# Kernel tuning notes

Hardware: AMD Instinct MI355X
Metric: run time of the kernel (lower is better)

## Reference

```python
import jax, jax.numpy as jnp
import numpy as np

B, T = 64, 512
D_CH, D_W = 50, 300
D_IN = D_CH + D_W          # 350, GRU input dim
H = 700                    # hidden_nums
U = H // 2                 # 350, units per direction


def _gru_dir(x, mask, Wx, Wh, b, reverse):
    """Keras GRU (reset_after=True, gate order z,r,h) over time axis.
    x: [B,T,D_IN], mask: [B,T] bool, Wx: [D_IN,3U], Wh: [U,3U], b: [2,3U].
    Masked steps carry the previous state (Keras masking semantics).
    Returns hidden states [B,T,U] aligned to input time order."""
    xg = jnp.einsum('btd,dg->btg', x, Wx) + b[0]  # [B,T,3U] precomputed input gates

    def step(h, inp):
        xg_t, m = inp                      # [B,3U], [B]
        hg = h @ Wh + b[1]                 # [B,3U]
        z = jax.nn.sigmoid(xg_t[:, :U] + hg[:, :U])
        r = jax.nn.sigmoid(xg_t[:, U:2 * U] + hg[:, U:2 * U])
        hh = jnp.tanh(xg_t[:, 2 * U:] + r * hg[:, 2 * U:])
        h_new = z * h + (1.0 - z) * hh
        h = jnp.where(m[:, None], h_new, h)
        return h, h

    h0 = jnp.zeros((x.shape[0], U), x.dtype)
    _, ys = jax.lax.scan(step, h0, (xg.transpose(1, 0, 2), mask.T), reverse=reverse)
    return ys.transpose(1, 0, 2)           # [B,T,U]


def setup_inputs() -> dict:
    key = jax.random.key(0)
    ks = jax.random.split(key, 12)
    char_embedding = jax.random.normal(ks[0], (B, T, D_CH), jnp.float32)
    word_embedding = jax.random.normal(ks[1], (B, T, D_W), jnp.float32)
    sequence_length = jax.random.randint(ks[2], (B,), 1, T + 1, jnp.int32)
    mask = jnp.arange(T)[None, :] < sequence_length[:, None]  # right-padded bool mask

    def glorot(k, shape):
        lim = np.sqrt(6.0 / (shape[0] + shape[1]))
        return jax.random.uniform(k, shape, jnp.float32, -lim, lim)

    W_z = glorot(ks[3], (2, H))
    W_q = glorot(ks[4], (2, H))
    Wx_f = glorot(ks[5], (D_IN, 3 * U))
    Wh_f = glorot(ks[6], (U, 3 * U))
    b_f = jnp.zeros((2, 3 * U), jnp.float32)
    Wx_b = glorot(ks[7], (D_IN, 3 * U))
    Wh_b = glorot(ks[8], (U, 3 * U))
    b_b = jnp.zeros((2, 3 * U), jnp.float32)
    return {
        'char_embedding': char_embedding, 'word_embedding': word_embedding,
        'sequence_length': sequence_length, 'mask': mask,
        'W_z': W_z, 'W_q': W_q,
        'Wx_f': Wx_f, 'Wh_f': Wh_f, 'b_f': b_f,
        'Wx_b': Wx_b, 'Wh_b': Wh_b, 'b_b': b_b,
    }


def reference(char_embedding, word_embedding, sequence_length, mask,
              W_z, W_q, Wx_f, Wh_f, b_f, Wx_b, Wh_b, b_b):
    x = jnp.concatenate([char_embedding, word_embedding], axis=-1)   # [B,T,350]
    h_fw = _gru_dir(x, mask, Wx_f, Wh_f, b_f, reverse=False)
    h_bw = _gru_dir(x, mask, Wx_b, Wh_b, b_b, reverse=True)
    hidden_states = jnp.concatenate([h_fw, h_bw], axis=-1)           # [B,T,700]
    z_T = jax.nn.softmax(jnp.einsum('bth,ch->btc', hidden_states, W_z), axis=-1)
    z_S = jax.nn.softmax(jnp.einsum('bth,ch->btc', hidden_states, W_q), axis=-1)
    return (z_T, z_S, hidden_states)
```

## Files before the change

kernel.cpp:

```cpp
#include <hip/hip_runtime.h>
#include <hip/hip_bf16.h>
#include <math.h>

#define BB   64
#define TT   512
#define UU   350
#define GG   1050
#define DCH  50
#define DWD  300
#define DIN  350
#define CT   64
#define NCH  8

#define NSLICE 22
#define UPB    16
#define NBG    4
#define BPG    16

#define FLAGS_OFF 0
#define WHT_ROW   352
#define WHT_OFF   1024
#define WHT_BYTES (2*GG*WHT_ROW*4)
#define XG_OFF    (WHT_OFF + WHT_BYTES)

__global__ __launch_bounds__(256) void wht_kernel(
    const float* __restrict__ Whf, const float* __restrict__ Whb,
    float* __restrict__ WhT)
{
    int idx = blockIdx.x * 256 + threadIdx.x;
    if (idx >= 2 * WHT_ROW * GG) return;
    int dir = idx / (WHT_ROW * GG);
    int r   = idx % (WHT_ROW * GG);
    int u   = r / GG;
    int g   = r % GG;
    const float* src = dir ? Whb : Whf;
    float v = (u < UU) ? src[u * GG + g] : 0.f;
    WhT[((size_t)dir * GG + g) * WHT_ROW + u] = v;
}

__global__ __launch_bounds__(256) void xg_gemm_kernel(
    const float* __restrict__ ce, const float* __restrict__ we,
    const float* __restrict__ Wxf, const float* __restrict__ Wxb,
    const float* __restrict__ bf,  const float* __restrict__ bb,
    float* __restrict__ xg, int c)
{
    const int dir   = blockIdx.z;
    const int tloc  = blockIdx.y;
    const int gbase = blockIdx.x * 64;
    const int t     = dir ? (448 - c * CT + tloc) : (c * CT + tloc);
    const float* __restrict__ Wx   = dir ? Wxb : Wxf;
    const float* __restrict__ bias = dir ? bb  : bf;

    __shared__ float xs[16][68];
    __shared__ float wsh[16][68];

    const int tid = threadIdx.x;
    const int b0 = (tid & 15) * 4;
    const int g0 = (tid >> 4) * 4;
    float acc[4][4] = {};

    for (int k0 = 0; k0 < DIN; k0 += 16) {
        #pragma unroll
        for (int j = 0; j < 4; ++j) {
            int e = j * 256 + tid;
            int bbi = e >> 4, kk = e & 15;
            int k = k0 + kk;
            float v = 0.f;
            if (k < DIN)
                v = (k < DCH) ? ce[((size_t)bbi * TT + t) * DCH + k]
                              : we[((size_t)bbi * TT + t) * DWD + (k - DCH)];
            xs[kk][bbi] = v;
        }
        #pragma unroll
        for (int j = 0; j < 4; ++j) {
            int e = j * 256 + tid;
            int kk = e >> 6, gg = e & 63;
            int k = k0 + kk, g = gbase + gg;
            float v = 0.f;
            if (k < DIN && g < GG) v = Wx[(size_t)k * GG + g];
            wsh[kk][gg] = v;
        }
        __syncthreads();
        #pragma unroll
        for (int kk = 0; kk < 16; ++kk) {
            float4 xa = *(const float4*)&xs[kk][b0];
            float4 wa = *(const float4*)&wsh[kk][g0];
            acc[0][0] = fmaf(wa.x, xa.x, acc[0][0]);
            acc[0][1] = fmaf(wa.x, xa.y, acc[0][1]);
            acc[0][2] = fmaf(wa.x, xa.z, acc[0][2]);
            acc[0][3] = fmaf(wa.x, xa.w, acc[0][3]);
            acc[1][0] = fmaf(wa.y, xa.x, acc[1][0]);
            acc[1][1] = fmaf(wa.y, xa.y, acc[1][1]);
            acc[1][2] = fmaf(wa.y, xa.z, acc[1][2]);
            acc[1][3] = fmaf(wa.y, xa.w, acc[1][3]);
            acc[2][0] = fmaf(wa.z, xa.x, acc[2][0]);
            acc[2][1] = fmaf(wa.z, xa.y, acc[2][1]);
            acc[2][2] = fmaf(wa.z, xa.z, acc[2][2]);
            acc[2][3] = fmaf(wa.z, xa.w, acc[2][3]);
            acc[3][0] = fmaf(wa.w, xa.x, acc[3][0]);
            acc[3][1] = fmaf(wa.w, xa.y, acc[3][1]);
            acc[3][2] = fmaf(wa.w, xa.z, acc[3][2]);
            acc[3][3] = fmaf(wa.w, xa.w, acc[3][3]);
        }
        __syncthreads();
    }
    float* outp = xg + (size_t)((dir * CT + tloc) * GG) * BB;
    #pragma unroll
    for (int i = 0; i < 4; ++i) {
        int g = gbase + g0 + i;
        if (g < GG) {
            float bv = bias[g];
            float4 v;
            v.x = acc[i][0] + bv; v.y = acc[i][1] + bv;
            v.z = acc[i][2] + bv; v.w = acc[i][3] + bv;
            *(float4*)&outp[(size_t)g * BB + b0] = v;
        }
    }
}

__global__ __launch_bounds__(256) void gru_chunk_kernel(
    const float* __restrict__ xg, const float* __restrict__ WhT,
    const float* __restrict__ bf, const float* __restrict__ bb,
    const int* __restrict__ seqlen, int* __restrict__ flags,
    float* __restrict__ hid, int c)
{
    __shared__ float h_lds[BPG][356];

    const int tid  = threadIdx.x;
    const int lane = tid & 63;
    const int wv   = tid >> 6;
    const int slot = (lane >> 4) & 3;
    const int b16  = lane & 15;
    const int us   = blockIdx.x;
    const int bg   = blockIdx.y;
    const int dir  = blockIdx.z;
    const int u    = us * UPB + wv * 4 + slot;
    const int b    = bg * BPG + b16;
    const bool act = (u < UU);
    const int uc   = act ? u : 0;
    const int slen = seqlen[b];

    const float* __restrict__ bias = dir ? bb : bf;
    const float* __restrict__ wzp = WhT + (size_t)(dir * GG + uc)          * WHT_ROW;
    const float* __restrict__ wrp = WhT + (size_t)(dir * GG + UU + uc)     * WHT_ROW;
    const float* __restrict__ whp = WhT + (size_t)(dir * GG + 2 * UU + uc) * WHT_ROW;
    const float b1z = bias[GG + uc];
    const float b1r = bias[GG + UU + uc];
    const float b1h = bias[GG + 2 * UU + uc];
    int* myflags = flags + (dir * NBG + bg) * NSLICE;

    const int sb = tid >> 4;
    const int sk = (tid & 15) * 2;

    for (int sl = 0; sl < CT; ++sl) {
        const int s = c * CT + sl;
        const int t = dir ? (TT - 1 - s) : s;

        if (s > 0) {
            for (;;) {
                int ok = 1;
                if (lane < NSLICE)
                    ok = (__hip_atomic_load(&myflags[lane], __ATOMIC_RELAXED,
                                            __HIP_MEMORY_SCOPE_AGENT) >= s);
                if (__all(ok)) break;
                __builtin_amdgcn_s_sleep(2);
            }
            const int tp = dir ? (t + 1) : (t - 1);
            const float* hrow = hid + ((size_t)(bg * BPG + sb) * TT + tp) * 700 + dir * UU;
            #pragma unroll
            for (int j = 0; j < 11; ++j) {
                int k0 = sk + 32 * j;
                if (k0 < UU) {
                    unsigned long long v = __hip_atomic_load(
                        (unsigned long long*)(hrow + k0),
                        __ATOMIC_RELAXED, __HIP_MEMORY_SCOPE_AGENT);
                    h_lds[sb][k0]     = __uint_as_float((unsigned)v);
                    h_lds[sb][k0 + 1] = __uint_as_float((unsigned)(v >> 32));
                }
            }
        }
        __syncthreads();

        float hz = b1z, hr = b1r, hcd = b1h;
        float hprev = 0.f;
        if (s > 0) {
            const float* hl = &h_lds[b16][0];
            #pragma unroll 3
            for (int k = 0; k < 348; k += 4) {
                float4 h4  = *(const float4*)(hl + k);
                float4 wz4 = *(const float4*)(wzp + k);
                float4 wr4 = *(const float4*)(wrp + k);
                float4 wh4 = *(const float4*)(whp + k);
                hz  = fmaf(h4.x, wz4.x, hz);
                hz  = fmaf(h4.y, wz4.y, hz);
                hz  = fmaf(h4.z, wz4.z, hz);
                hz  = fmaf(h4.w, wz4.w, hz);
                hr  = fmaf(h4.x, wr4.x, hr);
                hr  = fmaf(h4.y, wr4.y, hr);
                hr  = fmaf(h4.z, wr4.z, hr);
                hr  = fmaf(h4.w, wr4.w, hr);
                hcd = fmaf(h4.x, wh4.x, hcd);
                hcd = fmaf(h4.y, wh4.y, hcd);
                hcd = fmaf(h4.z, wh4.z, hcd);
                hcd = fmaf(h4.w, wh4.w, hcd);
            }
            float2 ht = *(const float2*)(hl + 348);
            hz  = fmaf(ht.x, wzp[348], hz);   hz  = fmaf(ht.y, wzp[349], hz);
            hr  = fmaf(ht.x, wrp[348], hr);   hr  = fmaf(ht.y, wrp[349], hr);
            hcd = fmaf(ht.x, whp[348], hcd);  hcd = fmaf(ht.y, whp[349], hcd);
            hprev = hl[uc];
        }

        const int tloc = dir ? (CT - 1 - sl) : sl;
        const float* xgp = xg + (size_t)((dir * CT + tloc) * GG) * BB;
        float xz = 0.f, xr = 0.f, xh = 0.f;
        if (act) {
            xz = xgp[(size_t)uc * BB + b];
            xr = xgp[(size_t)(uc + UU) * BB + b];
            xh = xgp[(size_t)(uc + 2 * UU) * BB + b];
        }
        float z   = 1.f / (1.f + expf(-(xz + hz)));
        float r   = 1.f / (1.f + expf(-(xr + hr)));
        float cnd = tanhf(xh + r * hcd);
        float hnew = z * hprev + (1.f - z) * cnd;
        hnew = (t < slen) ? hnew : hprev;

        if (act)
            __hip_atomic_store(&hid[((size_t)b * TT + t) * 700 + dir * UU + u], hnew,
                               __ATOMIC_RELAXED, __HIP_MEMORY_SCOPE_AGENT);

        asm volatile("s_waitcnt vmcnt(0)" ::: "memory");
        __syncthreads();
        if (tid == 0)
            __hip_atomic_store(&myflags[us], s + 1,
                               __ATOMIC_RELAXED, __HIP_MEMORY_SCOPE_AGENT);
    }
}

__global__ __launch_bounds__(256) void proj_kernel(
    const float* __restrict__ Wz, const float* __restrict__ Wq,
    const float* __restrict__ hid, float* __restrict__ zT, float* __restrict__ zS)
{
    const int wave = threadIdx.x >> 6;
    const int lane = threadIdx.x & 63;
    const int row  = blockIdx.x * 4 + wave;
    const float* hp = hid + (size_t)row * 700;
    float a0 = 0.f, a1 = 0.f, a2 = 0.f, a3 = 0.f;
    #pragma unroll
    for (int i = 0; i < 11; ++i) {
        int j = i * 64 + lane;
        if (j < 700) {
            float hv = hp[j];
            a0 = fmaf(hv, Wz[j], a0);
            a1 = fmaf(hv, Wz[700 + j], a1);
            a2 = fmaf(hv, Wq[j], a2);
            a3 = fmaf(hv, Wq[700 + j], a3);
        }
    }
    #pragma unroll
    for (int off = 32; off; off >>= 1) {
        a0 += __shfl_xor(a0, off, 64);
        a1 += __shfl_xor(a1, off, 64);
        a2 += __shfl_xor(a2, off, 64);
        a3 += __shfl_xor(a3, off, 64);
    }
    if (lane == 0) {
        float m1 = fmaxf(a0, a1);
        float e0 = expf(a0 - m1), e1 = expf(a1 - m1);
        float s1 = e0 + e1;
        zT[(size_t)row * 2]     = e0 / s1;
        zT[(size_t)row * 2 + 1] = e1 / s1;
        float m2 = fmaxf(a2, a3);
        float f0 = expf(a2 - m2), f1 = expf(a3 - m2);
        float s2 = f0 + f1;
        zS[(size_t)row * 2]     = f0 / s2;
        zS[(size_t)row * 2 + 1] = f1 / s2;
    }
}

extern "C" void kernel_launch(void* const* d_in, const int* in_sizes, int n_in,
                              void* d_out, int out_size, void* d_ws, size_t ws_size,
                              hipStream_t stream)
{
    (void)in_sizes; (void)n_in; (void)out_size; (void)ws_size;
    const float* ce  = (const float*)d_in[0];
    const float* we  = (const float*)d_in[1];
    const int*   sl  = (const int*)d_in[2];
    const float* Wz  = (const float*)d_in[4];
    const float* Wq  = (const float*)d_in[5];
    const float* Wxf = (const float*)d_in[6];
    const float* Whf = (const float*)d_in[7];
    const float* bf  = (const float*)d_in[8];
    const float* Wxb = (const float*)d_in[9];
    const float* Whb = (const float*)d_in[10];
    const float* bb  = (const float*)d_in[11];

    float* out = (float*)d_out;
    float* zT  = out;
    float* zS  = out + (size_t)BB * TT * 2;
    float* hid = out + (size_t)2 * BB * TT * 2;

    char* ws = (char*)d_ws;
    int*   flags = (int*)(ws + FLAGS_OFF);
    float* WhT   = (float*)(ws + WHT_OFF);
    float* xg    = (float*)(ws + XG_OFF);

    hipMemsetAsync(flags, 0, 1024, stream);
    wht_kernel<<<dim3((2 * WHT_ROW * GG + 255) / 256), 256, 0, stream>>>(Whf, Whb, WhT);

    int cvals[NCH];
    for (int c = 0; c < NCH; ++c) {
        xg_gemm_kernel<<<dim3(17, CT, 2), 256, 0, stream>>>(ce, we, Wxf, Wxb, bf, bb, xg, c);
        cvals[c] = c;
        const float* xgc = xg;
        const float* WhTc = WhT;
        void* args[] = { (void*)&xgc, (void*)&WhTc, (void*)&bf, (void*)&bb,
                         (void*)&sl, (void*)&flags, (void*)&hid, (void*)&cvals[c] };
        hipLaunchCooperativeKernel((const void*)gru_chunk_kernel,
                                   dim3(NSLICE, NBG, 2), dim3(256), args, 0, stream);
    }
    proj_kernel<<<dim3(BB * TT / 4), 256, 0, stream>>>(Wz, Wq, hid, zT, zS);
}
```

Baseline: 8.337 ms.

## Stage recurrent weights in LDS and split GRU across more slices

```diff
diff --git a/kernel.cpp b/kernel.cpp
--- a/kernel.cpp
+++ b/kernel.cpp
@@ -12,14 +12,14 @@
 #define CT   64
 #define NCH  8
 
-#define NSLICE 22
-#define UPB    16
+#define NSLICE 44
+#define UPB    8
 #define NBG    4
 #define BPG    16
 
 #define FLAGS_OFF 0
 #define WHT_ROW   352
-#define WHT_OFF   1024
+#define WHT_OFF   2048
 #define WHT_BYTES (2*GG*WHT_ROW*4)
 #define XG_OFF    (WHT_OFF + WHT_BYTES)
 
@@ -118,39 +118,54 @@
     }
 }
 
-__global__ __launch_bounds__(256) void gru_chunk_kernel(
+__global__ __launch_bounds__(128, 1) void gru_chunk_kernel(
     const float* __restrict__ xg, const float* __restrict__ WhT,
     const float* __restrict__ bf, const float* __restrict__ bb,
     const int* __restrict__ seqlen, int* __restrict__ flags,
     float* __restrict__ hid, int c)
 {
+    __shared__ float w_lds[UPB * 3 * 360];
     __shared__ float h_lds[BPG][356];
 
     const int tid  = threadIdx.x;
     const int lane = tid & 63;
-    const int wv   = tid >> 6;
-    const int slot = (lane >> 4) & 3;
-    const int b16  = lane & 15;
+    const int ul   = tid >> 4;
+    const int b16  = tid & 15;
     const int us   = blockIdx.x;
     const int bg   = blockIdx.y;
     const int dir  = blockIdx.z;
-    const int u    = us * UPB + wv * 4 + slot;
+    const int u    = us * UPB + ul;
     const int b    = bg * BPG + b16;
     const bool act = (u < UU);
     const int uc   = act ? u : 0;
     const int slen = seqlen[b];
 
     const float* __restrict__ bias = dir ? bb : bf;
-    const float* __restrict__ wzp = WhT + (size_t)(dir * GG + uc)          * WHT_ROW;
-    const float* __restrict__ wrp = WhT + (size_t)(dir * GG + UU + uc)     * WHT_ROW;
-    const float* __restrict__ whp = WhT + (size_t)(dir * GG + 2 * UU + uc) * WHT_ROW;
     const float b1z = bias[GG + uc];
     const float b1r = bias[GG + UU + uc];
     const float b1h = bias[GG + 2 * UU + uc];
     int* myflags = flags + (dir * NBG + bg) * NSLICE;
 
-    const int sb = tid >> 4;
-    const int sk = (tid & 15) * 2;
+    {
+        float4* wl4 = (float4*)w_lds;
+        for (int i = tid; i < UPB * 3 * 88; i += 128) {
+            int uu = i / (3 * 88);
+            int rem = i % (3 * 88);
+            int g = rem / 88;
+            int kq = rem % 88;
+            int ug = us * UPB + uu;
+            float4 v = make_float4(0.f, 0.f, 0.f, 0.f);
+            if (ug < UU)
+                v = *(const float4*)&WhT[((size_t)(dir * GG + g * UU + ug)) * WHT_ROW + kq * 4];
+            wl4[(uu * 3 + g) * 90 + kq] = v;
+        }
+    }
+    const float* __restrict__ wzp = &w_lds[(ul * 3 + 0) * 360];
+    const float* __restrict__ wrp = &w_lds[(ul * 3 + 1) * 360];
+    const float* __restrict__ whp = &w_lds[(ul * 3 + 2) * 360];
+
+    const int sb = tid >> 3;
+    const int sk = (tid & 7) * 2;
 
     for (int sl = 0; sl < CT; ++sl) {
         const int s = c * CT + sl;
@@ -163,13 +178,13 @@
                     ok = (__hip_atomic_load(&myflags[lane], __ATOMIC_RELAXED,
                                             __HIP_MEMORY_SCOPE_AGENT) >= s);
                 if (__all(ok)) break;
-                __builtin_amdgcn_s_sleep(2);
+                __builtin_amdgcn_s_sleep(1);
             }
             const int tp = dir ? (t + 1) : (t - 1);
             const float* hrow = hid + ((size_t)(bg * BPG + sb) * TT + tp) * 700 + dir * UU;
             #pragma unroll
-            for (int j = 0; j < 11; ++j) {
-                int k0 = sk + 32 * j;
+            for (int j = 0; j < 22; ++j) {
+                int k0 = sk + 16 * j;
                 if (k0 < UU) {
                     unsigned long long v = __hip_atomic_load(
                         (unsigned long long*)(hrow + k0),
@@ -181,11 +196,20 @@
         }
         __syncthreads();
 
+        const int tloc = dir ? (CT - 1 - sl) : sl;
+        const float* xgp = xg + (size_t)((dir * CT + tloc) * GG) * BB;
+        float xz = 0.f, xr = 0.f, xh = 0.f;
+        if (act) {
+            xz = xgp[(size_t)uc * BB + b];
+            xr = xgp[(size_t)(uc + UU) * BB + b];
+            xh = xgp[(size_t)(uc + 2 * UU) * BB + b];
+        }
+
         float hz = b1z, hr = b1r, hcd = b1h;
         float hprev = 0.f;
         if (s > 0) {
             const float* hl = &h_lds[b16][0];
-            #pragma unroll 3
+            #pragma unroll 8
             for (int k = 0; k < 348; k += 4) {
                 float4 h4  = *(const float4*)(hl + k);
                 float4 wz4 = *(const float4*)(wzp + k);
@@ -211,14 +235,6 @@
             hprev = hl[uc];
         }
 
-        const int tloc = dir ? (CT - 1 - sl) : sl;
-        const float* xgp = xg + (size_t)((dir * CT + tloc) * GG) * BB;
-        float xz = 0.f, xr = 0.f, xh = 0.f;
-        if (act) {
-            xz = xgp[(size_t)uc * BB + b];
-            xr = xgp[(size_t)(uc + UU) * BB + b];
-            xh = xgp[(size_t)(uc + 2 * UU) * BB + b];
-        }
         float z   = 1.f / (1.f + expf(-(xz + hz)));
         float r   = 1.f / (1.f + expf(-(xr + hr)));
         float cnd = tanhf(xh + r * hcd);
@@ -305,7 +321,7 @@
     float* WhT   = (float*)(ws + WHT_OFF);
     float* xg    = (float*)(ws + XG_OFF);
 
-    hipMemsetAsync(flags, 0, 1024, stream);
+    hipMemsetAsync(flags, 0, 2048, stream);
     wht_kernel<<<dim3((2 * WHT_ROW * GG + 255) / 256), 256, 0, stream>>>(Whf, Whb, WhT);
 
     int cvals[NCH];
@@ -317,7 +333,7 @@
         void* args[] = { (void*)&xgc, (void*)&WhTc, (void*)&bf, (void*)&bb,
                          (void*)&sl, (void*)&flags, (void*)&hid, (void*)&cvals[c] };
         hipLaunchCooperativeKernel((const void*)gru_chunk_kernel,
-                                   dim3(NSLICE, NBG, 2), dim3(256), args, 0, stream);
+                                   dim3(NSLICE, NBG, 2), dim3(128), args, 0, stream);
     }
     proj_kernel<<<dim3(BB * TT / 4), 256, 0, stream>>>(Wz, Wq, hid, zT, zS);
 }
```

Result: slower. 8.536 ms (+2.4%).
